# Kernel optimization log

Measured on AMD Instinct MI355X. Metric: run time of the kernel, lower is better.

Reference implementation:

```python
import jax, jax.numpy as jnp
import numpy as np
from jax import lax

NUM_SEGMENTS = 50
HIDDEN = 128
IN_CH = 64
LOGSIG_DIM = IN_CH + IN_CH * (IN_CH - 1) // 2 + IN_CH  # level1 + Levy area + startpoint


def setup_inputs() -> dict:
    key = jax.random.key(0)
    k0, k1, k2, k3, k4 = jax.random.split(key, 5)
    B, C, T, V = 16, IN_CH, 200, 25
    x = jax.random.normal(k0, (B, C, T, V), dtype=jnp.float32)
    s = 1.0 / np.sqrt(HIDDEN).astype(np.float32)
    W_ih = jax.random.uniform(k1, (4 * HIDDEN, LOGSIG_DIM), jnp.float32, -s, s)
    W_hh = jax.random.uniform(k2, (4 * HIDDEN, HIDDEN), jnp.float32, -s, s)
    b_ih = jax.random.uniform(k3, (4 * HIDDEN,), jnp.float32, -s, s)
    b_hh = jax.random.uniform(k4, (4 * HIDDEN,), jnp.float32, -s, s)
    return {"x": x, "W_ih": W_ih, "W_hh": W_hh, "b_ih": b_ih, "b_hh": b_hh}


def _segment_logsig(xn):
    # xn: (N, C, T). Split T into NUM_SEGMENTS chunks; level-2 log-signature per chunk.
    N, C, T = xn.shape
    L = T // NUM_SEGMENTS  # points per segment
    p = xn.transpose(0, 2, 1).reshape(N, NUM_SEGMENTS, L, C)  # path points
    start = p[:, :, 0]                                  # (N,S,C) segment startpoint
    inc = p[:, :, 1:] - p[:, :, :-1]                    # (N,S,L-1,C) increments
    dev = p[:, :, :-1] - start[:, :, None]              # (N,S,L-1,C) p_t - p_0
    # Level-2 iterated integrals (cross terms): S2_ij = sum_t dev_t,i * inc_t,j
    S2 = jnp.einsum('nsti,nstj->nsij', dev, inc)        # (N,S,C,C)
    A = 0.5 * (S2 - S2.transpose(0, 1, 3, 2))           # Levy area (antisymmetric part)
    iu, ju = jnp.triu_indices(C, k=1)
    levy = A[:, :, iu, ju]                              # (N,S,C(C-1)/2)
    lvl1 = p[:, :, -1] - start                          # (N,S,C) level-1 term
    return jnp.concatenate([lvl1, levy, start], axis=-1)  # (N,S,LOGSIG_DIM)


def _lstm(seq, W_ih, W_hh, b_ih, b_hh):
    # seq: (N, S, F). Single-layer unidirectional LSTM, torch gate order (i,f,g,o).
    N = seq.shape[0]
    x_proj = jnp.einsum('nsf,gf->nsg', seq, W_ih) + b_ih + b_hh  # (N,S,4H)

    def step(carry, xt):
        h, c = carry
        gates = xt + h @ W_hh.T
        i, f, g, o = jnp.split(gates, 4, axis=-1)
        c = jax.nn.sigmoid(f) * c + jax.nn.sigmoid(i) * jnp.tanh(g)
        h = jax.nn.sigmoid(o) * jnp.tanh(c)
        return (h, c), h

    h0 = jnp.zeros((N, HIDDEN), seq.dtype)
    c0 = jnp.zeros((N, HIDDEN), seq.dtype)
    _, hs = lax.scan(step, (h0, c0), x_proj.transpose(1, 0, 2))
    return hs.transpose(1, 0, 2)  # (N,S,H)


def reference(x, W_ih, W_hh, b_ih, b_hh):
    B, C, T, V = x.shape
    xn = x.transpose(0, 3, 1, 2).reshape(B * V, C, T)
    ls = _segment_logsig(xn)                      # (B*V, S, LOGSIG_DIM)
    h = _lstm(ls, W_ih, W_hh, b_ih, b_hh)          # (B*V, S, H)
    out = h.reshape(B, V, NUM_SEGMENTS, HIDDEN).transpose(0, 3, 2, 1)
    return out  # (B, H, S, V)
```

## Files before the change

kernel.cpp:

```cpp
#include <hip/hip_runtime.h>
#include <stdint.h>

#define NSEG 50
#define HID 128
#define KDIM 2144
#define KD2 2240
#define KD2B 4480
#define NROW 20000
#define NROW_PAD 20096
#define GATES 512
#define NSEQ 400
#define NGRP 528

typedef __attribute__((ext_vector_type(8))) _Float16 f16x8;
typedef __attribute__((ext_vector_type(4))) _Float16 f16x4;
typedef __attribute__((ext_vector_type(4))) float f32x4;
typedef __attribute__((ext_vector_type(4))) uint32_t u32x4;

#define GLB_SPACE __attribute__((address_space(1)))
#define LDS_SPACE __attribute__((address_space(3)))

__device__ __forceinline__ void g2lds16(const void* g, void* l) {
    __builtin_amdgcn_global_load_lds((const GLB_SPACE uint32_t*)g,
                                     (LDS_SPACE uint32_t*)l, 16, 0, 0);
}

__device__ __forceinline__ int goff528(int i) {
    int n = 63 - i;
    int q = n >> 2, t = n & 3;
    return NGRP - (q + 1) * (2 * q + t);
}
__device__ __forceinline__ int ifromg(int g) {
    int i = 63 - (int)sqrtf(8.0f * (float)(NGRP - g));
    if (i < 0) i = 0;
    if (i > 62) i = 62;
    while (i > 0 && goff528(i) > g) i--;
    while (goff528(i + 1) <= g) i++;
    return i;
}

#define UVP(c) ((((c) & 3) << 4) | ((c) >> 2))

__global__ __launch_bounds__(512) void feat_kernel(const float* __restrict__ x,
                                                   const float* __restrict__ Wih,
                                                   const float* __restrict__ Whh,
                                                   const float* __restrict__ bih,
                                                   const float* __restrict__ bhh,
                                                   _Float16* __restrict__ feat,
                                                   _Float16* __restrict__ wh,
                                                   _Float16* __restrict__ whh16,
                                                   float* __restrict__ bias) {
    int bid = blockIdx.x;
    int tid = threadIdx.x;

    __shared__ float pbuf[64 * 101];
    __shared__ __align__(16) float4 uv4[25 * 64];

    if (bid >= 800) {
        int* kmap = (int*)pbuf;
        for (int k = tid; k < KD2; k += 512) {
            int orig;
            if (k < 64) {
                orig = k;
            } else if (k < 64 + 4 * NGRP) {
                int g = (k - 64) >> 2, p = (k - 64) & 3;
                int i = ifromg(g);
                int j = i + 1 + 4 * (g - goff528(i)) + p;
                orig = (j < 64) ? (64 + 63 * i - (i * (i - 1)) / 2 + (j - i - 1)) : -1;
            } else {
                orig = 2080 + (k - (64 + 4 * NGRP));
            }
            kmap[k] = orig;
        }
        __syncthreads();
        const int nwih = 512 * KD2;
        const int nwhh = 512 * HID;
        const int total = nwih + nwhh + 512;
        for (int idx = (bid - 800) * 512 + tid; idx < total; idx += 64 * 512) {
            if (idx < nwih) {
                int row = idx / KD2;
                int k = idx - row * KD2;
                int orig = kmap[k];
                wh[idx] = (orig >= 0) ? (_Float16)Wih[row * KDIM + orig] : (_Float16)0.0f;
            } else if (idx < nwih + nwhh) {
                int q = idx - nwih;
                whh16[q] = (_Float16)Whh[q];
            } else {
                int g = idx - nwih - nwhh;
                bias[g] = bih[g] + bhh[g];
            }
        }
        return;
    }

    int b = bid / NSEG;
    int s = bid - b * NSEG;

    for (int i = tid; i < 6400; i += 512) {
        int c = i / 100;
        int r = i - c * 100;
        pbuf[c * 101 + r] = x[(((size_t)b * 64 + c) * 200 + 4 * s) * 25 + r];
    }
    __syncthreads();

    for (int i = tid; i < 1600; i += 512) {
        int v = i >> 6;
        int c = i & 63;
        float p0 = pbuf[c * 101 + v];
        float p1 = pbuf[c * 101 + 25 + v];
        float p2 = pbuf[c * 101 + 50 + v];
        float p3 = pbuf[c * 101 + 75 + v];
        uv4[v * 64 + UVP(c)] = make_float4(p1 - p0, p2 - p0, p2 - p1, p3 - p2);
        size_t m = ((size_t)(b * 25 + v)) * NSEG + s;
        feat[m * KD2 + c] = (_Float16)(p3 - p0);
        feat[m * KD2 + (64 + 4 * NGRP) + c] = (_Float16)p0;
    }
    __syncthreads();

    for (int idx = tid; idx < 4 * NGRP; idx += 512) {
        int vb = idx / NGRP;
        int g = idx - vb * NGRP;
        int i = ifromg(g);
        int t = g - goff528(i);
        int j0 = i + 1 + 4 * t;
        int k0 = 64 + 4 * g;
        float msk[4];
        int jc[4];
#pragma unroll
        for (int p = 0; p < 4; p++) {
            int j = j0 + p;
            msk[p] = (j < 64) ? 0.5f : 0.0f;
            jc[p] = (j < 64) ? UVP(j) : UVP(63);
        }
        int ip = UVP(i);
        int v0 = (vb == 0) ? 0 : 6 * vb + 1;
        int vn = (vb == 0) ? 7 : 6;
        for (int vv = 0; vv < vn; vv++) {
            int v = v0 + vv;
            const float4* rowv = &uv4[v * 64];
            float4 a = rowv[ip];
            f16x4 o;
#pragma unroll
            for (int p = 0; p < 4; p++) {
                float4 bb = rowv[jc[p]];
                float val = msk[p] * (a.x * bb.z - bb.x * a.z + a.y * bb.w - bb.y * a.w);
                o[p] = (_Float16)val;
            }
            size_t m = ((size_t)(b * 25 + v)) * NSEG + s;
            *(f16x4*)(feat + m * KD2 + k0) = o;
        }
    }
}

__global__ __launch_bounds__(256, 2) void gemm_kernel(const _Float16* __restrict__ feat,
                                                      const _Float16* __restrict__ wh,
                                                      const float* __restrict__ bias,
                                                      _Float16* __restrict__ xproj2) {
    int bid = blockIdx.x;
    int x = bid & 7;
    int t = bid >> 3;
    int nb = t & 3;
    int mt = (t >> 2) * 8 + x;
    if (mt >= 157) return;
    int m0 = mt * 128;
    int n0 = nb * 128;
    int tid = threadIdx.x;
    int wave = tid >> 6;
    int lane = tid & 63;
    int quad = lane >> 4;
    int l15 = lane & 15;
    int wm = (wave >> 1) * 64;
    int wn = (wave & 1) * 64;

    int r8 = lane >> 3;
    int gcol = ((lane & 7) * 16) ^ (r8 * 16);

    __shared__ __align__(16) _Float16 smem[2][16384];

    const f32x4 z4 = {0.f, 0.f, 0.f, 0.f};
    f32x4 acc[4][4];
    for (int i = 0; i < 4; i++)
        for (int j = 0; j < 4; j++) acc[i][j] = z4;

    const char* featB = (const char*)feat;
    const char* whB = (const char*)wh;

    const char* aSrc[4];
    const char* bSrc[4];
#pragma unroll
    for (int it = 0; it < 4; it++) {
        int rb = it * 32 + wave * 8;
        aSrc[it] = featB + (size_t)(m0 + rb + r8) * KD2B + gcol;
        bSrc[it] = whB + (size_t)(n0 + rb + r8) * KD2B + gcol;
    }

    {
        char* As = (char*)smem[0];
        char* Bs = (char*)smem[0] + 16384;
#pragma unroll
        for (int it = 0; it < 4; it++) {
            int rb = it * 32 + wave * 8;
            g2lds16(aSrc[it], As + rb * 128);
            g2lds16(bSrc[it], Bs + rb * 128);
        }
    }
    __syncthreads();

    for (int kt = 0; kt < 35; kt++) {
        int cur = kt & 1;
        if (kt + 1 < 35) {
            size_t kb = (size_t)(kt + 1) * 128;
            char* As = (char*)smem[cur ^ 1];
            char* Bs = (char*)smem[cur ^ 1] + 16384;
#pragma unroll
            for (int it = 0; it < 4; it++) {
                int rb = it * 32 + wave * 8;
                g2lds16(aSrc[it] + kb, As + rb * 128);
                g2lds16(bSrc[it] + kb, Bs + rb * 128);
            }
        }
        {
            const char* As = (const char*)smem[cur];
            const char* Bs = (const char*)smem[cur] + 16384;
            for (int ks = 0; ks < 2; ks++) {
                int off = ((ks * 64) | (quad * 16)) ^ ((l15 & 7) * 16);
                f16x8 af[4], bf[4];
                for (int tt = 0; tt < 4; tt++)
                    af[tt] = *(const f16x8*)(As + (wm + tt * 16 + l15) * 128 + off);
                for (int tt = 0; tt < 4; tt++)
                    bf[tt] = *(const f16x8*)(Bs + (wn + tt * 16 + l15) * 128 + off);
                for (int mtl = 0; mtl < 4; mtl++)
                    for (int ntl = 0; ntl < 4; ntl++)
                        acc[mtl][ntl] = __builtin_amdgcn_mfma_f32_16x16x32_f16(af[mtl], bf[ntl], acc[mtl][ntl], 0, 0, 0);
            }
        }
        __syncthreads();
    }

    _Float16* ep = (_Float16*)smem;
    for (int ntl = 0; ntl < 4; ntl++) {
        int nl = wn + ntl * 16 + l15;
        float bv = bias[n0 + nl];
        for (int mtl = 0; mtl < 4; mtl++)
            for (int r = 0; r < 4; r++) {
                int ml = wm + mtl * 16 + quad * 4 + r;
                ep[ml * 132 + nl] = (_Float16)(acc[mtl][ntl][r] + bv);
            }
    }
    __syncthreads();
    {
        int row = tid >> 1;
        int half = tid & 1;
        int m = m0 + row;
        if (m < NROW) {
            unsigned q = (unsigned)m / 50u;
            unsigned s = (unsigned)m - q * 50u;
            const char* src = (const char*)ep + row * 264 + half * 128;
            char* dst = (char*)xproj2 + ((size_t)s * NSEQ + q) * 1024 + (size_t)n0 * 2 + half * 128;
            for (int i = 0; i < 8; i++)
                *(u32x4*)(dst + i * 16) = *(const u32x4*)(src + i * 16);
        }
    }
}

__global__ __launch_bounds__(512, 2) void lstm_kernel(const _Float16* __restrict__ xproj2,
                                                      const _Float16* __restrict__ whh,
                                                      _Float16* __restrict__ hseq) {
    int bid = blockIdx.x;
    int tid = threadIdx.x;
    int wave = tid >> 6;
    int lane = tid & 63;
    int quad = lane >> 4;
    int col = lane & 15;
    int hid = wave * 16 + col;

    __shared__ __align__(16) char xbuf[25 * 4 * 1040];
    __shared__ __align__(16) _Float16 hst[NSEG * 4 * HID];
    __shared__ __align__(16) _Float16 hbuf[2][4 * 144];

    f16x8 bfrag[4][4];
    for (int g = 0; g < 4; g++) {
        int n = g * 128 + hid;
        for (int kq = 0; kq < 4; kq++)
            bfrag[g][kq] = *(const f16x8*)(whh + (size_t)n * HID + kq * 32 + quad * 8);
    }
    for (int i = tid; i < 2 * 4 * 144; i += 512) ((_Float16*)hbuf)[i] = (_Float16)0.0f;
    float cst = 0.0f;

    const char* xsrc = (const char*)xproj2;
    for (int r = wave; r < 100; r += 8)
        g2lds16(xsrc + ((size_t)((r >> 2) * NSEQ + bid * 4 + (r & 3))) * 1024 + lane * 16,
                xbuf + r * 1040);
    __syncthreads();

    const f32x4 z4 = {0.f, 0.f, 0.f, 0.f};
    for (int half = 0; half < 2; half++) {
        for (int ss = 0; ss < 25; ss++) {
            int s = half * 25 + ss;
            int cur = s & 1;
            int nxt = cur ^ 1;

            f16x8 afrag[4];
            for (int kq = 0; kq < 4; kq++)
                afrag[kq] = *(const f16x8*)(&hbuf[cur][(col & 3) * 144 + kq * 32 + quad * 8]);

            float xp[4];
            for (int g = 0; g < 4; g++)
                xp[g] = (float)(*(const _Float16*)(xbuf + (ss * 4 + quad) * 1040 +
                               (g * 128 + hid) * 2));

            f32x4 acc[4];
            for (int g = 0; g < 4; g++) {
                acc[g] = z4;
                for (int kq = 0; kq < 4; kq++)
                    acc[g] = __builtin_amdgcn_mfma_f32_16x16x32_f16(afrag[kq], bfrag[g][kq], acc[g], 0, 0, 0);
            }

            float gv[4];
            for (int g = 0; g < 4; g++) {
                float lo = (quad & 1) ? acc[g][1] : acc[g][0];
                float hi = (quad & 1) ? acc[g][3] : acc[g][2];
                gv[g] = (quad & 2) ? hi : lo;
            }

            float ip = gv[0] + xp[0];
            float fp = gv[1] + xp[1];
            float gp = gv[2] + xp[2];
            float op = gv[3] + xp[3];
            float si = __fdividef(1.0f, 1.0f + __expf(-ip));
            float sf = __fdividef(1.0f, 1.0f + __expf(-fp));
            float so = __fdividef(1.0f, 1.0f + __expf(-op));
            float eg = __expf(-2.0f * gp);
            float tg = __fdividef(1.0f - eg, 1.0f + eg);
            cst = sf * cst + si * tg;
            float ec = __expf(-2.0f * cst);
            float tc = __fdividef(1.0f - ec, 1.0f + ec);
            float hv = so * tc;
            _Float16 hv16 = (_Float16)hv;
            hbuf[nxt][quad * 144 + hid] = hv16;
            hst[(s * 4 + quad) * 128 + hid] = hv16;
            __syncthreads();
        }
        if (half == 0) {
            for (int r = wave; r < 100; r += 8)
                g2lds16(xsrc + ((size_t)((25 + (r >> 2)) * NSEQ + bid * 4 + (r & 3))) * 1024 + lane * 16,
                        xbuf + r * 1040);
            __syncthreads();
        }
    }

    const u32x4* src = (const u32x4*)hst;
    for (int i = tid; i < 3200; i += 512) {
        int s = i >> 6;
        int rem = i & 63;
        int seq = rem >> 4;
        int seg = rem & 15;
        u32x4 v = src[i];
        *(u32x4*)((char*)hseq + ((size_t)(s * NSEQ + bid * 4 + seq)) * 256 + seg * 16) = v;
    }
}

__global__ __launch_bounds__(256) void tr_kernel(const _Float16* __restrict__ hseq,
                                                 float* __restrict__ out) {
    int bid = blockIdx.x;
    int b = bid / NSEG;
    int s = bid - b * NSEG;
    int tid = threadIdx.x;

    __shared__ _Float16 buf[25 * 130];

    const uint32_t* src32 = (const uint32_t*)(hseq + ((size_t)s * NSEQ + b * 25) * HID);
    uint32_t* buf32 = (uint32_t*)buf;
    for (int i = tid; i < 1600; i += 256) {
        int v = i >> 6;
        int d = i & 63;
        buf32[v * 65 + d] = src32[i];
    }
    __syncthreads();
    for (int i = tid; i < 3200; i += 256) {
        int hid = i / 25;
        int v = i - hid * 25;
        out[(((size_t)b * 128 + hid) * NSEG + s) * 25 + v] = (float)buf[v * 130 + hid];
    }
}

extern "C" void kernel_launch(void* const* d_in, const int* in_sizes, int n_in,
                              void* d_out, int out_size, void* d_ws, size_t ws_size,
                              hipStream_t stream) {
    const float* x = (const float*)d_in[0];
    const float* Wih = (const float*)d_in[1];
    const float* Whh = (const float*)d_in[2];
    const float* bih = (const float*)d_in[3];
    const float* bhh = (const float*)d_in[4];
    float* out = (float*)d_out;

    char* ws = (char*)d_ws;
    size_t off = 0;
    _Float16* feat = (_Float16*)(ws + off);   off += (size_t)NROW_PAD * KD2 * 2;
    _Float16* xproj2 = (_Float16*)(ws + off); off += (size_t)NSEG * NSEQ * GATES * 2;
    _Float16* hseq = (_Float16*)(ws + off);   off += (size_t)NSEG * NSEQ * HID * 2;
    _Float16* wh = (_Float16*)(ws + off);     off += (size_t)512 * KD2 * 2;
    _Float16* whh16 = (_Float16*)(ws + off);  off += (size_t)512 * HID * 2;
    float* bias = (float*)(ws + off);         off += 512 * 4;

    hipLaunchKernelGGL(feat_kernel, dim3(864), dim3(512), 0, stream,
                       x, Wih, Whh, bih, bhh, feat, wh, whh16, bias);
    hipLaunchKernelGGL(gemm_kernel, dim3(640), dim3(256), 0, stream, feat, wh, bias, xproj2);
    hipLaunchKernelGGL(lstm_kernel, dim3(100), dim3(512), 0, stream, xproj2, whh16, hseq);
    hipLaunchKernelGGL(tr_kernel, dim3(16 * NSEG), dim3(256), 0, stream, hseq, out);
}
```

Before: 226.4 us.

## Enlarge GEMM tile to 256x256 with 512-thread blocks and two-pass epilogue

```diff
diff --git a/kernel.cpp b/kernel.cpp
--- a/kernel.cpp
+++ b/kernel.cpp
@@ -7,7 +7,7 @@
 #define KD2 2240
 #define KD2B 4480
 #define NROW 20000
-#define NROW_PAD 20096
+#define NROW_PAD 20224
 #define GATES 512
 #define NSEQ 400
 #define NGRP 528
@@ -152,35 +152,32 @@
     }
 }
 
-__global__ __launch_bounds__(256, 2) void gemm_kernel(const _Float16* __restrict__ feat,
+__global__ __launch_bounds__(512, 2) void gemm_kernel(const _Float16* __restrict__ feat,
                                                       const _Float16* __restrict__ wh,
                                                       const float* __restrict__ bias,
                                                       _Float16* __restrict__ xproj2) {
     int bid = blockIdx.x;
-    int x = bid & 7;
-    int t = bid >> 3;
-    int nb = t & 3;
-    int mt = (t >> 2) * 8 + x;
-    if (mt >= 157) return;
-    int m0 = mt * 128;
-    int n0 = nb * 128;
+    int mt = bid >> 1;
+    int nb = bid & 1;
+    int m0 = mt * 256;
+    int n0 = nb * 256;
     int tid = threadIdx.x;
     int wave = tid >> 6;
     int lane = tid & 63;
     int quad = lane >> 4;
     int l15 = lane & 15;
     int wm = (wave >> 1) * 64;
-    int wn = (wave & 1) * 64;
+    int wn = (wave & 1) * 128;
 
     int r8 = lane >> 3;
     int gcol = ((lane & 7) * 16) ^ (r8 * 16);
 
-    __shared__ __align__(16) _Float16 smem[2][16384];
+    __shared__ __align__(16) char smem[2][65536];
 
     const f32x4 z4 = {0.f, 0.f, 0.f, 0.f};
-    f32x4 acc[4][4];
+    f32x4 acc[4][8];
     for (int i = 0; i < 4; i++)
-        for (int j = 0; j < 4; j++) acc[i][j] = z4;
+        for (int j = 0; j < 8; j++) acc[i][j] = z4;
 
     const char* featB = (const char*)feat;
     const char* whB = (const char*)wh;
@@ -189,17 +186,17 @@
     const char* bSrc[4];
 #pragma unroll
     for (int it = 0; it < 4; it++) {
-        int rb = it * 32 + wave * 8;
+        int rb = it * 64 + wave * 8;
         aSrc[it] = featB + (size_t)(m0 + rb + r8) * KD2B + gcol;
         bSrc[it] = whB + (size_t)(n0 + rb + r8) * KD2B + gcol;
     }
 
     {
-        char* As = (char*)smem[0];
-        char* Bs = (char*)smem[0] + 16384;
+        char* As = smem[0];
+        char* Bs = smem[0] + 32768;
 #pragma unroll
         for (int it = 0; it < 4; it++) {
-            int rb = it * 32 + wave * 8;
+            int rb = it * 64 + wave * 8;
             g2lds16(aSrc[it], As + rb * 128);
             g2lds16(bSrc[it], Bs + rb * 128);
         }
@@ -208,29 +205,29 @@
 
     for (int kt = 0; kt < 35; kt++) {
         int cur = kt & 1;
-        if (kt + 1 < 35) {
+        if (kt < 34) {
             size_t kb = (size_t)(kt + 1) * 128;
-            char* As = (char*)smem[cur ^ 1];
-            char* Bs = (char*)smem[cur ^ 1] + 16384;
+            char* As = smem[cur ^ 1];
+            char* Bs = smem[cur ^ 1] + 32768;
 #pragma unroll
             for (int it = 0; it < 4; it++) {
-                int rb = it * 32 + wave * 8;
+                int rb = it * 64 + wave * 8;
                 g2lds16(aSrc[it] + kb, As + rb * 128);
                 g2lds16(bSrc[it] + kb, Bs + rb * 128);
             }
         }
         {
-            const char* As = (const char*)smem[cur];
-            const char* Bs = (const char*)smem[cur] + 16384;
+            const char* As = smem[cur];
+            const char* Bs = smem[cur] + 32768;
             for (int ks = 0; ks < 2; ks++) {
                 int off = ((ks * 64) | (quad * 16)) ^ ((l15 & 7) * 16);
-                f16x8 af[4], bf[4];
+                f16x8 af[4], bf[8];
                 for (int tt = 0; tt < 4; tt++)
                     af[tt] = *(const f16x8*)(As + (wm + tt * 16 + l15) * 128 + off);
-                for (int tt = 0; tt < 4; tt++)
+                for (int tt = 0; tt < 8; tt++)
                     bf[tt] = *(const f16x8*)(Bs + (wn + tt * 16 + l15) * 128 + off);
                 for (int mtl = 0; mtl < 4; mtl++)
-                    for (int ntl = 0; ntl < 4; ntl++)
+                    for (int ntl = 0; ntl < 8; ntl++)
                         acc[mtl][ntl] = __builtin_amdgcn_mfma_f32_16x16x32_f16(af[mtl], bf[ntl], acc[mtl][ntl], 0, 0, 0);
             }
         }
@@ -238,28 +235,31 @@
     }
 
     _Float16* ep = (_Float16*)smem;
-    for (int ntl = 0; ntl < 4; ntl++) {
-        int nl = wn + ntl * 16 + l15;
-        float bv = bias[n0 + nl];
-        for (int mtl = 0; mtl < 4; mtl++)
-            for (int r = 0; r < 4; r++) {
-                int ml = wm + mtl * 16 + quad * 4 + r;
-                ep[ml * 132 + nl] = (_Float16)(acc[mtl][ntl][r] + bv);
-            }
-    }
-    __syncthreads();
-    {
-        int row = tid >> 1;
-        int half = tid & 1;
-        int m = m0 + row;
-        if (m < NROW) {
-            unsigned q = (unsigned)m / 50u;
-            unsigned s = (unsigned)m - q * 50u;
-            const char* src = (const char*)ep + row * 264 + half * 128;
-            char* dst = (char*)xproj2 + ((size_t)s * NSEQ + q) * 1024 + (size_t)n0 * 2 + half * 128;
-            for (int i = 0; i < 8; i++)
-                *(u32x4*)(dst + i * 16) = *(const u32x4*)(src + i * 16);
-        }
+    for (int p = 0; p < 2; p++) {
+        if ((wave >> 2) == p) {
+            for (int ntl = 0; ntl < 8; ntl++) {
+                int nl = wn + ntl * 16 + l15;
+                float bv = bias[n0 + nl];
+                for (int mtl = 0; mtl < 4; mtl++)
+                    for (int r = 0; r < 4; r++) {
+                        int relm = wm - p * 128 + mtl * 16 + quad * 4 + r;
+                        ep[relm * 260 + nl] = (_Float16)(acc[mtl][ntl][r] + bv);
+                    }
+            }
+        }
+        __syncthreads();
+        for (int it = 0; it < 8; it++) {
+            int rowp = it * 16 + (tid >> 5);
+            int m = m0 + p * 128 + rowp;
+            if (m < NROW) {
+                unsigned q = (unsigned)m / 50u;
+                unsigned s = (unsigned)m - q * 50u;
+                const char* src = (const char*)ep + rowp * 520 + (tid & 31) * 16;
+                char* dst = (char*)xproj2 + ((size_t)s * NSEQ + q) * 1024 + (size_t)n0 * 2 + (tid & 31) * 16;
+                *(u32x4*)dst = *(const u32x4*)src;
+            }
+        }
+        __syncthreads();
     }
 }
 
@@ -405,7 +405,7 @@
 
     hipLaunchKernelGGL(feat_kernel, dim3(864), dim3(512), 0, stream,
                        x, Wih, Whh, bih, bhh, feat, wh, whh16, bias);
-    hipLaunchKernelGGL(gemm_kernel, dim3(640), dim3(256), 0, stream, feat, wh, bias, xproj2);
+    hipLaunchKernelGGL(gemm_kernel, dim3(158), dim3(512), 0, stream, feat, wh, bias, xproj2);
     hipLaunchKernelGGL(lstm_kernel, dim3(100), dim3(512), 0, stream, xproj2, whh16, hseq);
     hipLaunchKernelGGL(tr_kernel, dim3(16 * NSEG), dim3(256), 0, stream, hseq, out);
 }
```

After: 214.4 us. -5.3%, faster.
